# Kernel optimization log

Hardware: AMD Instinct MI355X
Metric: run time of the kernel (lower is better)

The kernel has to match this reference:

```python
import jax, jax.numpy as jnp
import numpy as np

N = 100000      # nodes
E = 1600000     # directed edges (avg degree 16)
F_IN = 128      # in_channels
H = 128         # hidden
G = 64          # graphs in batch


def setup_inputs() -> dict:
    key = jax.random.key(0)
    ks = jax.random.split(key, 9)
    x = jax.random.normal(ks[0], (N, F_IN), dtype=jnp.float32)
    edge_index = jax.random.randint(ks[1], (2, E), 0, N, dtype=jnp.int32)
    batch = jnp.sort(jax.random.randint(ks[2], (N,), 0, G, dtype=jnp.int32))
    # GCNConv weights (glorot-ish scale) and biases
    W1 = jax.random.normal(ks[3], (F_IN, H), dtype=jnp.float32) / np.sqrt(F_IN)
    b1 = jnp.zeros((H,), dtype=jnp.float32)
    W2 = jax.random.normal(ks[4], (H, H // 2), dtype=jnp.float32) / np.sqrt(H)
    b2 = jnp.zeros((H // 2,), dtype=jnp.float32)
    lin_w = jax.random.normal(ks[5], (H // 2, 1), dtype=jnp.float32) / np.sqrt(H // 2)
    lin_b = jnp.zeros((1,), dtype=jnp.float32)
    return {"x": x, "edge_index": edge_index, "batch": batch,
            "W1": W1, "b1": b1, "W2": W2, "b2": b2,
            "lin_w": lin_w, "lin_b": lin_b}


def reference(x, edge_index, batch, W1, b1, W2, b2, lin_w, lin_b):
    n = x.shape[0]
    # GCN default: add self-loops, symmetric deg^-1/2 normalization
    loop = jnp.arange(n, dtype=edge_index.dtype)
    src = jnp.concatenate([edge_index[0], loop])
    dst = jnp.concatenate([edge_index[1], loop])
    deg = jax.ops.segment_sum(jnp.ones_like(dst, dtype=x.dtype), dst, num_segments=n)
    dis = jax.lax.rsqrt(jnp.maximum(deg, 1.0))  # deg >= 1 due to self-loops
    norm = dis[src] * dis[dst]                  # [E+N]

    def gcn_conv(h, W, b):
        h = h @ W                               # transform first (smaller dim on edges)
        m = h[src] * norm[:, None]              # gather + scale  [E+N, d]
        return jax.ops.segment_sum(m, dst, num_segments=n) + b  # scatter-add

    h = jax.nn.relu(gcn_conv(x, W1, b1))        # dropout = identity in eval mode
    h = jax.nn.relu(gcn_conv(h, W2, b2))

    # global_mean_pool over graph ids
    sums = jax.ops.segment_sum(h, batch, num_segments=G)            # [G, H//2]
    cnt = jax.ops.segment_sum(jnp.ones((n,), h.dtype), batch, num_segments=G)
    pooled = sums / jnp.maximum(cnt, 1.0)[:, None]

    return (pooled @ lin_w + lin_b)[:, 0]       # squeeze(-1) -> [G]
```

## Files before the change

kernel.cpp:

```cpp
#include <hip/hip_runtime.h>
#include <hip/hip_fp16.h>


#define DN 512
#define DSHIFT 9
#define SLOT 80

typedef _Float16 half8 __attribute__((ext_vector_type(8)));
typedef _Float16 half4v __attribute__((ext_vector_type(4)));
typedef float f32x4 __attribute__((ext_vector_type(4)));

__global__ __launch_bounds__(1024) void k_split(
    const int* __restrict__ src, const int* __restrict__ dst,
    int* __restrict__ hcnt, int* __restrict__ binned, int E, int NBK, int PB,
    int CAPB, const float* __restrict__ W1, const float* __restrict__ W2,
    _Float16* __restrict__ W1t, _Float16* __restrict__ W2t) {
  __shared__ int h[256];
  int t = threadIdx.x;
  int b = blockIdx.x;
  if (b >= PB) {
    if (b == PB) {
      for (int i = t; i < 128 * 128; i += 1024)
        W1t[(i & 127) * 128 + (i >> 7)] = (_Float16)W1[i];
    } else {
      for (int i = t; i < 128 * 64; i += 1024)
        W2t[(i & 63) * 128 + (i >> 6)] = (_Float16)W2[i];
    }
    return;
  }
  if (t < 256) h[t] = 0;
  __syncthreads();
  int base = b * 8192;
  int pk[8], bk[8];
  bool val[8];
#pragma unroll
  for (int j = 0; j < 8; ++j) {
    int i = base + j * 1024 + t;
    val[j] = (i < E);
    if (val[j]) {
      int s = src[i], d = dst[i];
      bk[j] = d >> DSHIFT;
      pk[j] = (s << DSHIFT) | (d & (DN - 1));
      atomicAdd(&h[bk[j]], 1);
    }
  }
  __syncthreads();
  for (int k = t; k < NBK; k += 1024) hcnt[k * PB + b] = min(h[k], SLOT);
  __syncthreads();
  if (t < 256) h[t] = 0;
  __syncthreads();
#pragma unroll
  for (int j = 0; j < 8; ++j) {
    if (val[j]) {
      int slot = atomicAdd(&h[bk[j]], 1);
      if (slot < SLOT) binned[bk[j] * CAPB + b * SLOT + slot] = pk[j];
    }
  }
}

__global__ __launch_bounds__(1024) void k_bucket(const int* __restrict__ binned,
                                                 const int* __restrict__ hcnt,
                                                 int2* __restrict__ rr,
                                                 float* __restrict__ dis,
                                                 int* __restrict__ esrc,
                                                 int N, int PB, int CAPB) {
  __shared__ int hc[1024];
  __shared__ int lcnt[DN];
  __shared__ int lscan[DN];
  int k = blockIdx.x;
  int t = threadIdx.x;
  int nbase = k << DSHIFT;
  for (int b2 = t; b2 < PB; b2 += 1024) hc[b2] = hcnt[k * PB + b2];
  if (t < DN) lcnt[t] = 0;
  __syncthreads();
  for (int idx = t; idx < CAPB; idx += 1024) {
    int b2 = idx / SLOT, j = idx - b2 * SLOT;
    if (j < hc[b2])
      atomicAdd(&lcnt[binned[k * CAPB + idx] & (DN - 1)], 1);
  }
  __syncthreads();
  if (t < DN) lscan[t] = lcnt[t];
  __syncthreads();
  for (int off = 1; off < DN; off <<= 1) {
    int v = (t < DN && t >= off) ? lscan[t - off] : 0;
    __syncthreads();
    if (t < DN) lscan[t] += v;
    __syncthreads();
  }
  int bstart = k * CAPB;
  if (t < DN) {
    int g = nbase + t;
    if (g < N) {
      int inc = lscan[t];
      int c = lcnt[t];
      rr[g] = make_int2(bstart + inc - c, bstart + inc);
      dis[g] = rsqrtf((float)(c + 1));
    }
    lcnt[t] = lscan[t] - lcnt[t];
  }
  __syncthreads();
  for (int idx = t; idx < CAPB; idx += 1024) {
    int b2 = idx / SLOT, j = idx - b2 * SLOT;
    if (j < hc[b2]) {
      int p = binned[k * CAPB + idx];
      int slot = atomicAdd(&lcnt[p & (DN - 1)], 1);
      esrc[bstart + slot] = (unsigned)p >> DSHIFT;
    }
  }
}

template <int COLS, int K, typename AT, bool SCALE>
__global__ __launch_bounds__(256) void k_gemm(const AT* __restrict__ A,
                                              const _Float16* __restrict__ Wt_g,
                                              const float* __restrict__ dis,
                                              __half* __restrict__ out,
                                              int nrows) {
  constexpr int KP = K + 8;
  __shared__ _Float16 As[64 * KP];
  __shared__ _Float16 Wt[COLS * KP];
  int t = threadIdx.x;
  int row0 = blockIdx.x * 64;

  {
    constexpr int K8 = K / 8;
    for (int i = t; i < COLS * K8; i += 256) {
      int c = i / K8, k8 = (i % K8) * 8;
      *(half8*)&Wt[c * KP + k8] = *(const half8*)&Wt_g[c * K + k8];
    }
  }
  if constexpr (sizeof(AT) == 4) {
    constexpr int F4 = K / 4;
    for (int id = t; id < 64 * F4; id += 256) {
      int r = id / F4, kq = (id % F4) * 4;
      int grow = row0 + r;
      float4 av = (grow < nrows) ? *(const float4*)&A[(size_t)grow * K + kq]
                                 : make_float4(0.f, 0.f, 0.f, 0.f);
      half4v hv = {(_Float16)av.x, (_Float16)av.y, (_Float16)av.z,
                   (_Float16)av.w};
      *(half4v*)&As[r * KP + kq] = hv;
    }
  } else {
    constexpr int H8 = K / 8;
    for (int id = t; id < 64 * H8; id += 256) {
      int r = id / H8, kq = (id % H8) * 8;
      int grow = row0 + r;
      half8 av = (grow < nrows)
                     ? *(const half8*)&A[(size_t)grow * K + kq]
                     : (half8){0, 0, 0, 0, 0, 0, 0, 0};
      *(half8*)&As[r * KP + kq] = av;
    }
  }
  __syncthreads();

  int wave = t >> 6, lane = t & 63;
  int m = lane & 15;
  int quad = lane >> 4;
  constexpr int NT = COLS / 16;

  f32x4 acc[NT];
#pragma unroll
  for (int ct = 0; ct < NT; ++ct) acc[ct] = (f32x4){0.f, 0.f, 0.f, 0.f};

  const _Float16* arow = &As[(wave * 16 + m) * KP + quad * 8];
#pragma unroll
  for (int ks = 0; ks < K; ks += 32) {
    half8 af = *(const half8*)&arow[ks];
#pragma unroll
    for (int ct = 0; ct < NT; ++ct) {
      half8 bf = *(const half8*)&Wt[(ct * 16 + m) * KP + quad * 8 + ks];
      acc[ct] = __builtin_amdgcn_mfma_f32_16x16x32_f16(af, bf, acc[ct], 0, 0, 0);
    }
  }

  __syncthreads();
  _Float16* Ds = As;
  constexpr int DP = COLS + 4;
#pragma unroll
  for (int j = 0; j < 4; ++j) {
    int rl = wave * 16 + quad * 4 + j;
    int gr = row0 + rl;
    float dn = 1.f;
    if constexpr (SCALE) dn = (gr < nrows) ? dis[gr] : 0.f;
#pragma unroll
    for (int ct = 0; ct < NT; ++ct)
      Ds[rl * DP + ct * 16 + m] = (_Float16)(acc[ct][j] * dn);
  }
  __syncthreads();
  constexpr int C8 = COLS / 8;
  for (int id = t; id < 64 * C8; id += 256) {
    int r = id / C8, c8 = (id % C8) * 8;
    int gr = row0 + r;
    if (gr < nrows)
      *(half8*)&out[(size_t)gr * COLS + c8] = *(const half8*)&Ds[r * DP + c8];
  }
}

template <int COLS, bool FUSE>
__global__ __launch_bounds__(256) void k_agg(const __half* __restrict__ H,
                                             const int2* __restrict__ rr,
                                             const int* __restrict__ esrc,
                                             const float* __restrict__ dis,
                                             const float* __restrict__ bias,
                                             __half* __restrict__ out,
                                             const float* __restrict__ lin_w,
                                             float* __restrict__ dnode, int n) {
  constexpr int LPE = COLS / 8;
  constexpr int NG = 64 / LPE;
  int node = (blockIdx.x * 256 + threadIdx.x) >> 6;
  if (node >= n) return;
  int lane = threadIdx.x & 63;
  int group = lane / LPE;
  int c = (lane % LPE) * 8;

  float acc[8];
#pragma unroll
  for (int j = 0; j < 8; ++j) acc[j] = 0.f;

  int2 be = rr[node];
  int end = be.y;
  int e0 = be.x + group;
  int e1 = e0 + NG;
  int s0 = 0, s1 = 0;
  float w0 = 0.f, w1 = 0.f;
  if (e0 < end) { s0 = esrc[e0]; w0 = 1.f; }
  if (e1 < end) { s1 = esrc[e1]; w1 = 1.f; }
  while (e0 < end) {
    float4 r0 = *(const float4*)&H[(size_t)s0 * COLS + c];
    float4 r1 = *(const float4*)&H[(size_t)s1 * COLS + c];
    int e2 = e0 + 2 * NG, e3 = e1 + 2 * NG;
    int s2 = 0, s3 = 0;
    float w2 = 0.f, w3 = 0.f;
    if (e2 < end) { s2 = esrc[e2]; w2 = 1.f; }
    if (e3 < end) { s3 = esrc[e3]; w3 = 1.f; }
    {
      union { float4 f4; __half2 h2[4]; } u;
      u.f4 = r0;
#pragma unroll
      for (int j = 0; j < 4; ++j) {
        float2 f = __half22float2(u.h2[j]);
        acc[2 * j + 0] = fmaf(f.x, w0, acc[2 * j + 0]);
        acc[2 * j + 1] = fmaf(f.y, w0, acc[2 * j + 1]);
      }
      u.f4 = r1;
#pragma unroll
      for (int j = 0; j < 4; ++j) {
        float2 f = __half22float2(u.h2[j]);
        acc[2 * j + 0] = fmaf(f.x, w1, acc[2 * j + 0]);
        acc[2 * j + 1] = fmaf(f.y, w1, acc[2 * j + 1]);
      }
    }
    e0 = e2; s0 = s2; w0 = w2;
    e1 = e3; s1 = s3; w1 = w3;
  }
#pragma unroll
  for (int m = LPE; m < 64; m <<= 1) {
#pragma unroll
    for (int j = 0; j < 8; ++j) acc[j] += __shfl_xor(acc[j], m, 64);
  }
  if (group == 0) {
    float dn = dis[node];
    union { float4 f4; __half2 h2[4]; } u;
    u.f4 = *(const float4*)&H[(size_t)node * COLS + c];
    float o[8];
#pragma unroll
    for (int j = 0; j < 4; ++j) {
      float2 f = __half22float2(u.h2[j]);
      o[2 * j + 0] = fmaxf(fmaf(acc[2 * j + 0] + f.x, dn, bias[c + 2 * j + 0]), 0.f);
      o[2 * j + 1] = fmaxf(fmaf(acc[2 * j + 1] + f.y, dn, bias[c + 2 * j + 1]), 0.f);
    }
    if constexpr (FUSE) {
      float part = 0.f;
#pragma unroll
      for (int j = 0; j < 8; ++j) part = fmaf(o[j], lin_w[c + j], part);
      part += __shfl_xor(part, 1, 64);
      part += __shfl_xor(part, 2, 64);
      part += __shfl_xor(part, 4, 64);
      if (lane == 0) dnode[node] = part;
    } else {
      union { __half2 h2[4]; float4 f4; } ov;
#pragma unroll
      for (int j = 0; j < 4; ++j)
        ov.h2[j] = __floats2half2_rn(o[2 * j + 0], o[2 * j + 1]);
      *(float4*)&out[(size_t)node * COLS + c] = ov.f4;
    }
  }
}

__device__ inline int lower_bound_i(const int* a, int n, int v) {
  int lo = 0, hi = n;
  while (lo < hi) {
    int m = (lo + hi) >> 1;
    if (a[m] < v) lo = m + 1; else hi = m;
  }
  return lo;
}

__global__ __launch_bounds__(256) void k_poolfinal(const float* __restrict__ dnode,
                                                   const int* __restrict__ batch,
                                                   const float* __restrict__ lin_b,
                                                   float* __restrict__ out, int N) {
  __shared__ int bounds[2];
  __shared__ float red[4];
  int g = blockIdx.x;
  int t = threadIdx.x;
  if (t == 0) bounds[0] = lower_bound_i(batch, N, g);
  if (t == 1) bounds[1] = lower_bound_i(batch, N, g + 1);
  __syncthreads();
  int lo = bounds[0], hi = bounds[1];
  float s = 0.f;
  for (int i = lo + t; i < hi; i += 256) s += dnode[i];
#pragma unroll
  for (int m = 1; m < 64; m <<= 1) s += __shfl_xor(s, m, 64);
  if ((t & 63) == 0) red[t >> 6] = s;
  __syncthreads();
  if (t == 0) {
    float sum = red[0] + red[1] + red[2] + red[3];
    float cnt = (float)(hi - lo);
    out[g] = sum / fmaxf(cnt, 1.f) + lin_b[0];
  }
}

extern "C" void kernel_launch(void* const* d_in, const int* in_sizes, int n_in,
                              void* d_out, int out_size, void* d_ws, size_t ws_size,
                              hipStream_t stream) {
  const float* x = (const float*)d_in[0];
  const int* edge = (const int*)d_in[1];
  const int* batch = (const int*)d_in[2];
  const float* W1 = (const float*)d_in[3];
  const float* b1 = (const float*)d_in[4];
  const float* W2 = (const float*)d_in[5];
  const float* b2 = (const float*)d_in[6];
  const float* lin_w = (const float*)d_in[7];
  const float* lin_b = (const float*)d_in[8];
  float* out = (float*)d_out;

  const int N = in_sizes[2];
  const int E = in_sizes[1] / 2;
  const int G = out_size;
  const int* esrc_in = edge;
  const int* edst_in = edge + E;

  char* w = (char*)d_ws;
  size_t off = 0;
  auto take = [&](size_t bytes) {
    void* p = w + off;
    off += (bytes + 255) & ~(size_t)255;
    return p;
  };
  const int NBK = (N + DN - 1) / DN;
  const int PB = (E + 8191) / 8192;
  const int CAPB = PB * SLOT;
  int* hcnt = (int*)take((size_t)NBK * PB * 4);
  int2* rr = (int2*)take((size_t)N * 8);
  float* dis = (float*)take((size_t)N * 4);
  int* esrc = (int*)take((size_t)NBK * CAPB * 4);
  __half* XW = (__half*)take((size_t)N * 128 * 2);
  __half* H = (__half*)take((size_t)N * 128 * 2);
  float* dnode = (float*)take((size_t)N * 4);
  _Float16* W1t = (_Float16*)take((size_t)128 * 128 * 2);
  _Float16* W2t = (_Float16*)take((size_t)64 * 128 * 2);
  int* binned = (int*)H;
  (void)ws_size;
  (void)n_in;

  int GB = (N + 63) / 64;
  int ab = (int)(((size_t)N * 64 + 255) / 256);

  k_split<<<PB + 2, 1024, 0, stream>>>(esrc_in, edst_in, hcnt, binned, E, NBK,
                                       PB, CAPB, W1, W2, W1t, W2t);
  k_bucket<<<NBK, 1024, 0, stream>>>(binned, hcnt, rr, dis, esrc, N, PB, CAPB);
  k_gemm<128, 128, float, true><<<GB, 256, 0, stream>>>(x, W1t, dis, XW, N);
  k_agg<128, false><<<ab, 256, 0, stream>>>(XW, rr, esrc, dis, b1, H, nullptr,
                                            nullptr, N);
  k_gemm<64, 128, _Float16, true><<<GB, 256, 0, stream>>>(
      (const _Float16*)H, W2t, dis, XW, N);
  k_agg<64, true><<<ab, 256, 0, stream>>>(XW, rr, esrc, dis, b2, nullptr,
                                          lin_w, dnode, N);
  k_poolfinal<<<G, 256, 0, stream>>>(dnode, batch, lin_b, out, N);
}
```

Before: 278.5 us.

## Fuse layer-1 aggregation with layer-2 GEMM and swizzle blocks across XCDs

New measurement: 272.0 us, median of 2. 2.4% less time.

```diff
diff --git a/kernel.cpp b/kernel.cpp
--- a/kernel.cpp
+++ b/kernel.cpp
@@ -9,6 +9,12 @@
 typedef _Float16 half8 __attribute__((ext_vector_type(8)));
 typedef _Float16 half4v __attribute__((ext_vector_type(4)));
 typedef float f32x4 __attribute__((ext_vector_type(4)));
+
+__device__ __forceinline__ int xcd_swz(int b, int n) {
+  int x = b & 7, i = b >> 3;
+  int q = n >> 3, r = n & 7;
+  return x * q + min(x, r) + i;
+}
 
 __global__ __launch_bounds__(1024) void k_split(
     const int* __restrict__ src, const int* __restrict__ dst,
@@ -195,6 +201,133 @@
   }
 }
 
+__global__ __launch_bounds__(256) void k_aggemm(
+    const __half* __restrict__ XW, const int2* __restrict__ rr,
+    const int* __restrict__ esrc, const float* __restrict__ dis,
+    const float* __restrict__ bias, const _Float16* __restrict__ W2t,
+    __half* __restrict__ XW2, int N) {
+  constexpr int K = 128, KP = K + 8, COLS = 64, NT = COLS / 16;
+  __shared__ _Float16 As[64 * KP];
+  int t = threadIdx.x;
+  int lane = t & 63, wave = t >> 6;
+  int bid = xcd_swz((int)blockIdx.x, (int)gridDim.x);
+  int row0 = bid * 64;
+
+  int group = lane >> 4;
+  int c = (lane & 15) * 8;
+
+  for (int i = 0; i < 16; ++i) {
+    int r = wave * 16 + i;
+    int node = row0 + r;
+    float acc[8];
+#pragma unroll
+    for (int j = 0; j < 8; ++j) acc[j] = 0.f;
+    if (node < N) {
+      int2 be = rr[node];
+      int end = be.y;
+      int e0 = be.x + group;
+      int e1 = e0 + 4;
+      int s0 = 0, s1 = 0;
+      float w0 = 0.f, w1 = 0.f;
+      if (e0 < end) { s0 = esrc[e0]; w0 = 1.f; }
+      if (e1 < end) { s1 = esrc[e1]; w1 = 1.f; }
+      while (e0 < end) {
+        float4 r0 = *(const float4*)&XW[(size_t)s0 * 128 + c];
+        float4 r1 = *(const float4*)&XW[(size_t)s1 * 128 + c];
+        int e2 = e0 + 8, e3 = e1 + 8;
+        int s2 = 0, s3 = 0;
+        float w2 = 0.f, w3 = 0.f;
+        if (e2 < end) { s2 = esrc[e2]; w2 = 1.f; }
+        if (e3 < end) { s3 = esrc[e3]; w3 = 1.f; }
+        {
+          union { float4 f4; __half2 h2[4]; } u;
+          u.f4 = r0;
+#pragma unroll
+          for (int j = 0; j < 4; ++j) {
+            float2 f = __half22float2(u.h2[j]);
+            acc[2 * j + 0] = fmaf(f.x, w0, acc[2 * j + 0]);
+            acc[2 * j + 1] = fmaf(f.y, w0, acc[2 * j + 1]);
+          }
+          u.f4 = r1;
+#pragma unroll
+          for (int j = 0; j < 4; ++j) {
+            float2 f = __half22float2(u.h2[j]);
+            acc[2 * j + 0] = fmaf(f.x, w1, acc[2 * j + 0]);
+            acc[2 * j + 1] = fmaf(f.y, w1, acc[2 * j + 1]);
+          }
+        }
+        e0 = e2; s0 = s2; w0 = w2;
+        e1 = e3; s1 = s3; w1 = w3;
+      }
+#pragma unroll
+      for (int mm = 16; mm < 64; mm <<= 1) {
+#pragma unroll
+        for (int j = 0; j < 8; ++j) acc[j] += __shfl_xor(acc[j], mm, 64);
+      }
+    }
+    if (group == 0) {
+      half8 hv = (half8){0, 0, 0, 0, 0, 0, 0, 0};
+      if (node < N) {
+        float dn = dis[node];
+        union { float4 f4; __half2 h2[4]; } u;
+        u.f4 = *(const float4*)&XW[(size_t)node * 128 + c];
+        _Float16* hp = (_Float16*)&hv;
+#pragma unroll
+        for (int j = 0; j < 4; ++j) {
+          float2 f = __half22float2(u.h2[j]);
+          hp[2 * j + 0] =
+              (_Float16)fmaxf(fmaf(acc[2 * j + 0] + f.x, dn, bias[c + 2 * j + 0]), 0.f);
+          hp[2 * j + 1] =
+              (_Float16)fmaxf(fmaf(acc[2 * j + 1] + f.y, dn, bias[c + 2 * j + 1]), 0.f);
+        }
+      }
+      *(half8*)&As[r * KP + c] = hv;
+    }
+  }
+  __syncthreads();
+
+  int m = lane & 15, quad = lane >> 4;
+  half8 bfr[4][NT];
+#pragma unroll
+  for (int ks4 = 0; ks4 < 4; ++ks4)
+#pragma unroll
+    for (int ct = 0; ct < NT; ++ct)
+      bfr[ks4][ct] =
+          *(const half8*)&W2t[(ct * 16 + m) * K + ks4 * 32 + quad * 8];
+
+  f32x4 acc2[NT];
+#pragma unroll
+  for (int ct = 0; ct < NT; ++ct) acc2[ct] = (f32x4){0.f, 0.f, 0.f, 0.f};
+  const _Float16* arow = &As[(wave * 16 + m) * KP + quad * 8];
+#pragma unroll
+  for (int ks4 = 0; ks4 < 4; ++ks4) {
+    half8 af = *(const half8*)&arow[ks4 * 32];
+#pragma unroll
+    for (int ct = 0; ct < NT; ++ct)
+      acc2[ct] =
+          __builtin_amdgcn_mfma_f32_16x16x32_f16(af, bfr[ks4][ct], acc2[ct], 0, 0, 0);
+  }
+  __syncthreads();
+  _Float16* Ds = As;
+  constexpr int DP = COLS + 4;
+#pragma unroll
+  for (int j = 0; j < 4; ++j) {
+    int rl = wave * 16 + quad * 4 + j;
+    int gr = row0 + rl;
+    float dn = (gr < N) ? dis[gr] : 0.f;
+#pragma unroll
+    for (int ct = 0; ct < NT; ++ct)
+      Ds[rl * DP + ct * 16 + m] = (_Float16)(acc2[ct][j] * dn);
+  }
+  __syncthreads();
+  for (int id = t; id < 64 * 8; id += 256) {
+    int r = id / 8, c8 = (id % 8) * 8;
+    int gr = row0 + r;
+    if (gr < N)
+      *(half8*)&XW2[(size_t)gr * COLS + c8] = *(const half8*)&Ds[r * DP + c8];
+  }
+}
+
 template <int COLS, bool FUSE>
 __global__ __launch_bounds__(256) void k_agg(const __half* __restrict__ H,
                                              const int2* __restrict__ rr,
@@ -206,7 +339,8 @@
                                              float* __restrict__ dnode, int n) {
   constexpr int LPE = COLS / 8;
   constexpr int NG = 64 / LPE;
-  int node = (blockIdx.x * 256 + threadIdx.x) >> 6;
+  int bid = xcd_swz((int)blockIdx.x, (int)gridDim.x);
+  int node = (bid * 256 + (int)threadIdx.x) >> 6;
   if (node >= n) return;
   int lane = threadIdx.x & 63;
   int group = lane / LPE;
@@ -355,11 +489,11 @@
   float* dis = (float*)take((size_t)N * 4);
   int* esrc = (int*)take((size_t)NBK * CAPB * 4);
   __half* XW = (__half*)take((size_t)N * 128 * 2);
-  __half* H = (__half*)take((size_t)N * 128 * 2);
+  __half* XW2 = (__half*)take((size_t)N * 64 * 2);
   float* dnode = (float*)take((size_t)N * 4);
   _Float16* W1t = (_Float16*)take((size_t)128 * 128 * 2);
   _Float16* W2t = (_Float16*)take((size_t)64 * 128 * 2);
-  int* binned = (int*)H;
+  int* binned = (int*)XW2;
   (void)ws_size;
   (void)n_in;
 
@@ -370,11 +504,8 @@
                                        PB, CAPB, W1, W2, W1t, W2t);
   k_bucket<<<NBK, 1024, 0, stream>>>(binned, hcnt, rr, dis, esrc, N, PB, CAPB);
   k_gemm<128, 128, float, true><<<GB, 256, 0, stream>>>(x, W1t, dis, XW, N);
-  k_agg<128, false><<<ab, 256, 0, stream>>>(XW, rr, esrc, dis, b1, H, nullptr,
-                                            nullptr, N);
-  k_gemm<64, 128, _Float16, true><<<GB, 256, 0, stream>>>(
-      (const _Float16*)H, W2t, dis, XW, N);
-  k_agg<64, true><<<ab, 256, 0, stream>>>(XW, rr, esrc, dis, b2, nullptr,
+  k_aggemm<<<GB, 256, 0, stream>>>(XW, rr, esrc, dis, b1, W2t, XW2, N);
+  k_agg<64, true><<<ab, 256, 0, stream>>>(XW2, rr, esrc, dis, b2, nullptr,
                                           lin_w, dnode, N);
   k_poolfinal<<<G, 256, 0, stream>>>(dnode, batch, lin_b, out, N);
 }
```
